# Kernel tuning notes

Hardware: AMD Instinct MI355X
Metric: run time of the kernel (lower is better)

The kernel has to match this reference:

```python
import jax, jax.numpy as jnp
import numpy as np

DIM = 1024
NUM_HEADS = 16


def setup_inputs() -> dict:
    key = jax.random.key(0)
    ks = jax.random.split(key, 7)
    B, N, C = 2, 2048, DIM
    s = 1.0 / np.sqrt(C)
    x = jax.random.normal(ks[0], (B, N, C), dtype=jnp.float32)
    Wq = jax.random.normal(ks[1], (C, C), dtype=jnp.float32) * s
    Wk = jax.random.normal(ks[2], (C, C), dtype=jnp.float32) * s
    Wv = jax.random.normal(ks[3], (C, C), dtype=jnp.float32) * s
    bq = jnp.zeros((C,), dtype=jnp.float32)
    bk = jnp.zeros((C,), dtype=jnp.float32)
    bv = jnp.zeros((C,), dtype=jnp.float32)
    return {"x": x, "Wq": Wq, "bq": bq, "Wk": Wk, "bk": bk, "Wv": Wv, "bv": bv}


def reference(x, Wq, bq, Wk, bk, Wv, bv):
    B, N, C = x.shape
    H = NUM_HEADS
    D = C // H
    # Linear projections (torch Linear: x @ W.T + b)
    q = (x @ Wq.T + bq).reshape(B, N, H, D).transpose(0, 2, 1, 3)  # [B,H,N,D]
    k = (x @ Wk.T + bk).reshape(B, N, H, D).transpose(0, 2, 1, 3)
    v = (x @ Wv.T + bv).reshape(B, N, H, D).transpose(0, 2, 1, 3)
    # NOTE: original scales by sqrt(dim)=sqrt(C), not sqrt(head_dim)
    scale = 1.0 / np.sqrt(C).astype(np.float32)
    logits = jnp.einsum('bhnd,bhmd->bhnm', q, k) * scale  # [B,H,N,N]
    attn = jax.nn.softmax(logits, axis=-1)
    out = jnp.einsum('bhnm,bhmd->bhnd', attn, v)  # [B,H,N,D]
    return out.transpose(0, 2, 1, 3).reshape(B, N, C)
```

## Files before the change

### kernel.cpp

```cpp
#include <hip/hip_runtime.h>

typedef __attribute__((ext_vector_type(8))) short bf16x8;
typedef __attribute__((ext_vector_type(4))) float f32x4;
typedef __attribute__((ext_vector_type(16))) float f32x16;
typedef __attribute__((ext_vector_type(8))) unsigned short us8;
typedef unsigned short u16;
typedef unsigned int u32;

__device__ inline u16 f2bf(float f) {
  union { float f; unsigned u; } v; v.f = f;
  unsigned r = v.u + 0x7FFFu + ((v.u >> 16) & 1u);
  return (u16)(r >> 16);
}

__device__ inline u32 cvtpk_bf16(float lo, float hi) {
  u32 r;
  asm volatile("v_cvt_pk_bf16_f32 %0, %1, %2" : "=v"(r) : "v"(lo), "v"(hi));
  return r;
}

__device__ inline void gload_lds16(const void* g, void* l) {
  __builtin_amdgcn_global_load_lds(
      (const __attribute__((address_space(1))) void*)g,
      (__attribute__((address_space(3))) void*)l, 16, 0, 0);
}

__device__ inline void p_to_pf(const f32x16& p, bf16x8& f0, bf16x8& f1) {
  union { u32 u[4]; bf16x8 v; } fr;
  u32 a = cvtpk_bf16(p[0], p[1]),   c = cvtpk_bf16(p[2], p[3]);
  u32 b = cvtpk_bf16(p[4], p[5]),   d = cvtpk_bf16(p[6], p[7]);
  asm volatile("v_permlane32_swap_b32 %0, %1" : "+v"(a), "+v"(b));
  asm volatile("v_permlane32_swap_b32 %0, %1" : "+v"(c), "+v"(d));
  fr.u[0] = a; fr.u[1] = c; fr.u[2] = b; fr.u[3] = d;  f0 = fr.v;
  u32 a2 = cvtpk_bf16(p[8], p[9]),   c2 = cvtpk_bf16(p[10], p[11]);
  u32 b2 = cvtpk_bf16(p[12], p[13]), d2 = cvtpk_bf16(p[14], p[15]);
  asm volatile("v_permlane32_swap_b32 %0, %1" : "+v"(a2), "+v"(b2));
  asm volatile("v_permlane32_swap_b32 %0, %1" : "+v"(c2), "+v"(d2));
  fr.u[0] = a2; fr.u[1] = c2; fr.u[2] = b2; fr.u[3] = d2;  f1 = fr.v;
}

__global__ void cvt_all(const float* __restrict__ x, const float* __restrict__ wq,
                        const float* __restrict__ wk, const float* __restrict__ wv,
                        u16* __restrict__ out) {
  int i = (blockIdx.x * blockDim.x + threadIdx.x) * 4;
  const float* src; int off;
  if (i < 4194304)      { src = x;  off = 0; }
  else if (i < 5242880) { src = wq; off = 4194304; }
  else if (i < 6291456) { src = wk; off = 5242880; }
  else                  { src = wv; off = 6291456; }
  float4 v = *reinterpret_cast<const float4*>(src + (i - off));
  ushort4 o;
  o.x = f2bf(v.x); o.y = f2bf(v.y); o.z = f2bf(v.z); o.w = f2bf(v.w);
  *reinterpret_cast<ushort4*>(out + i) = o;
}

__global__ __launch_bounds__(256, 3) void gemm_qkv(
    const u16* __restrict__ X,
    const u16* __restrict__ Wq, const u16* __restrict__ Wk, const u16* __restrict__ Wv,
    const float* __restrict__ bq, const float* __restrict__ bk, const float* __restrict__ bv,
    u16* __restrict__ Oq, u16* __restrict__ Ok, u16* __restrict__ Ovt)
{
  constexpr int GK = 1024;
  __shared__ __align__(16) u16 As[128 * 64];
  __shared__ __align__(16) u16 Bs[128 * 64];

  const int z = blockIdx.z;
  const u16* W = (z == 0) ? Wq : (z == 1) ? Wk : Wv;
  const float* bias = (z == 0) ? bq : (z == 1) ? bk : bv;
  const float scale = (z == 0) ? (1.4426950408889634f / 32.0f) : 1.0f;

  const int tid = threadIdx.x;
  const int lane = tid & 63, w = tid >> 6;
  const int wm = w >> 1, wn = w & 1;
  const int q = lane & 15, g = lane >> 4;
  const int bm0 = blockIdx.x * 128, bn0 = blockIdx.y * 128;

  int srow[4], sgc[4];
  #pragma unroll
  for (int i = 0; i < 4; ++i) {
    int c = i * 256 + tid;
    srow[i] = c >> 3;
    sgc[i] = (((c & 7) ^ ((c >> 3) & 7)) * 8);
  }

  f32x4 acc[4][4];
  #pragma unroll
  for (int i = 0; i < 4; ++i)
    #pragma unroll
    for (int j = 0; j < 4; ++j) acc[i][j] = (f32x4){0.f, 0.f, 0.f, 0.f};

  for (int k0 = 0; k0 < GK; k0 += 64) {
    #pragma unroll
    for (int i = 0; i < 4; ++i) {
      int c8 = (i * 256 + tid) * 8;
      gload_lds16(&X[(bm0 + srow[i]) * GK + k0 + sgc[i]], &As[c8]);
      gload_lds16(&W[(bn0 + srow[i]) * GK + k0 + sgc[i]], &Bs[c8]);
    }
    __syncthreads();

    #pragma unroll
    for (int kk = 0; kk < 2; ++kk) {
      bf16x8 af[4], bfr[4];
      #pragma unroll
      for (int mi = 0; mi < 4; ++mi) {
        int row = wm * 64 + mi * 16 + q;
        af[mi] = *reinterpret_cast<const bf16x8*>(
            &As[row * 64 + (((kk * 4 + g) ^ (row & 7)) * 8)]);
      }
      #pragma unroll
      for (int ni = 0; ni < 4; ++ni) {
        int row = wn * 64 + ni * 16 + q;
        bfr[ni] = *reinterpret_cast<const bf16x8*>(
            &Bs[row * 64 + (((kk * 4 + g) ^ (row & 7)) * 8)]);
      }
      #pragma unroll
      for (int mi = 0; mi < 4; ++mi)
        #pragma unroll
        for (int ni = 0; ni < 4; ++ni)
          acc[mi][ni] = __builtin_amdgcn_mfma_f32_16x16x32_bf16(af[mi], bfr[ni], acc[mi][ni], 0, 0, 0);
    }
    __syncthreads();
  }

  if (z == 2) {
    #pragma unroll
    for (int mi = 0; mi < 4; ++mi) {
      #pragma unroll
      for (int ni = 0; ni < 4; ++ni) {
        int col = bn0 + wn * 64 + ni * 16 + q;
        float bb = bias[col];
        int h = col >> 6, d = col & 63;
        int row0 = bm0 + wm * 64 + mi * 16 + 4 * g;
        int b = row0 >> 11, n0 = row0 & 2047;
        ushort4 o4;
        o4.x = f2bf(acc[mi][ni][0] + bb);
        o4.y = f2bf(acc[mi][ni][1] + bb);
        o4.z = f2bf(acc[mi][ni][2] + bb);
        o4.w = f2bf(acc[mi][ni][3] + bb);
        *reinterpret_cast<ushort4*>(&Ovt[(((b << 4) + h) * 64 + d) * 2048 + n0]) = o4;
      }
    }
  } else {
    u16* O = (z == 0) ? Oq : Ok;
    #pragma unroll
    for (int mi = 0; mi < 4; ++mi) {
      #pragma unroll
      for (int ni = 0; ni < 4; ++ni) {
        int col = bn0 + wn * 64 + ni * 16 + q;
        float bb = bias[col];
        int h = col >> 6, d = col & 63;
        #pragma unroll
        for (int r = 0; r < 4; ++r) {
          int row = bm0 + wm * 64 + mi * 16 + 4 * g + r;
          int b = row >> 11, n = row & 2047;
          float v = (acc[mi][ni][r] + bb) * scale;
          O[(((b << 4) + h) * 2048 + n) * 64 + d] = f2bf(v);
        }
      }
    }
  }
}

__global__ __launch_bounds__(256, 2) void attn_kernel(
    const u16* __restrict__ Q, const u16* __restrict__ K, const u16* __restrict__ Vt,
    float* __restrict__ out)
{
  __shared__ __align__(16) u16 smem[32768];

  const int tid = threadIdx.x;
  const int lane = tid & 63, w = tid >> 6;
  const int half = w >> 1, qw = w & 1;
  const int th128 = (qw << 6) + lane;
  const int ql = lane & 31, h = lane >> 5, l7 = lane & 7;

  const int lin = blockIdx.x;
  const int xcd = lin & 7, li = lin >> 3;
  const int bh = xcd * 4 + (li >> 4);
  const int b = bh >> 4, hd = bh & 15;
  const int qrow0 = (li & 15) * 128 + qw * 64;

  const u16* Qp = Q + (bh * 2048 + qrow0) * 64;
  const u16* Kp = K + (bh * 2048 + half * 1024) * 64;
  const u16* Vp = Vt + bh * 64 * 2048 + half * 1024;

  bf16x8 qf[2][4];
  #pragma unroll
  for (int qh = 0; qh < 2; ++qh)
    #pragma unroll
    for (int ks = 0; ks < 4; ++ks)
      qf[qh][ks] = *reinterpret_cast<const bf16x8*>(Qp + (qh * 32 + ql) * 64 + 16 * ks + 8 * h);

  int srow[4], scb[4];
  #pragma unroll
  for (int i = 0; i < 4; ++i) {
    int c = i * 128 + th128;
    srow[i] = c >> 3;
    scb[i] = 16 * ((c & 7) ^ ((c >> 3) & 7));
  }

  u16* Kh = smem + half * 16384;
  u16* Vh = Kh + 8192;

  f32x16 o00, o01, o10, o11;
  #pragma unroll
  for (int i = 0; i < 16; ++i) { o00[i] = 0.f; o01[i] = 0.f; o10[i] = 0.f; o11[i] = 0.f; }
  float ls0 = 0.0f, ls1 = 0.0f;

  {
    #pragma unroll
    for (int i = 0; i < 4; ++i) {
      int c8 = (i * 128 + th128) * 8;
      gload_lds16((const char*)(Kp + srow[i] * 64) + scb[i], &Kh[c8]);
      gload_lds16((const char*)(Vp + srow[i] * 2048) + scb[i], &Vh[c8]);
    }
    __syncthreads();
  }

  for (int t = 0; t < 16; ++t) {
    const int cur = t & 1, nxt = cur ^ 1;
    if (t < 15) {
      const int kbn = t * 64 + 64;
      #pragma unroll
      for (int i = 0; i < 4; ++i) {
        int c8 = (i * 128 + th128) * 8;
        gload_lds16((const char*)(Kp + (kbn + srow[i]) * 64) + scb[i], &Kh[nxt * 4096 + c8]);
        gload_lds16((const char*)(Vp + srow[i] * 2048 + kbn) + scb[i], &Vh[nxt * 4096 + c8]);
      }
    }

    f32x16 p00, p01, p10, p11;
    #pragma unroll
    for (int i = 0; i < 16; ++i) { p00[i] = 0.f; p01[i] = 0.f; p10[i] = 0.f; p11[i] = 0.f; }
    const u16* kl = Kh + cur * 4096;
    __builtin_amdgcn_s_setprio(1);
    #pragma unroll
    for (int ks = 0; ks < 4; ++ks) {
      int cb = (16 * ks + 8 * h) ^ (l7 << 3);
      bf16x8 kf0 = *reinterpret_cast<const bf16x8*>(kl + ql * 64 + cb);
      p00 = __builtin_amdgcn_mfma_f32_32x32x16_bf16(kf0, qf[0][ks], p00, 0, 0, 0);
      p01 = __builtin_amdgcn_mfma_f32_32x32x16_bf16(kf0, qf[1][ks], p01, 0, 0, 0);
      bf16x8 kf1 = *reinterpret_cast<const bf16x8*>(kl + (32 + ql) * 64 + cb);
      p10 = __builtin_amdgcn_mfma_f32_32x32x16_bf16(kf1, qf[0][ks], p10, 0, 0, 0);
      p11 = __builtin_amdgcn_mfma_f32_32x32x16_bf16(kf1, qf[1][ks], p11, 0, 0, 0);
    }
    __builtin_amdgcn_s_setprio(0);

    const u16* vl = Vh + cur * 4096;
    bf16x8 vfa[4];
    #pragma unroll
    for (int sl = 0; sl < 4; ++sl) {
      int cb = (16 * sl + 8 * h) ^ (l7 << 3);
      vfa[sl] = *reinterpret_cast<const bf16x8*>(vl + ql * 64 + cb);
    }

    #pragma unroll
    for (int i = 0; i < 16; ++i) {
      p00[i] = __builtin_amdgcn_exp2f(p00[i]);
      p01[i] = __builtin_amdgcn_exp2f(p01[i]);
      p10[i] = __builtin_amdgcn_exp2f(p10[i]);
      p11[i] = __builtin_amdgcn_exp2f(p11[i]);
    }
    {
      float s0 = 0.f, s1 = 0.f;
      #pragma unroll
      for (int i = 0; i < 16; ++i) { s0 += p00[i] + p10[i]; s1 += p01[i] + p11[i]; }
      s0 += __shfl_xor(s0, 32);
      s1 += __shfl_xor(s1, 32);
      ls0 += s0; ls1 += s1;
    }

    bf16x8 pf[4][2];
    p_to_pf(p00, pf[0][0], pf[1][0]);
    p_to_pf(p10, pf[2][0], pf[3][0]);
    p_to_pf(p01, pf[0][1], pf[1][1]);
    p_to_pf(p11, pf[2][1], pf[3][1]);

    __builtin_amdgcn_s_setprio(1);
    #pragma unroll
    for (int sl = 0; sl < 4; ++sl) {
      o00 = __builtin_amdgcn_mfma_f32_32x32x16_bf16(vfa[sl], pf[sl][0], o00, 0, 0, 0);
      o01 = __builtin_amdgcn_mfma_f32_32x32x16_bf16(vfa[sl], pf[sl][1], o01, 0, 0, 0);
      int cb = (16 * sl + 8 * h) ^ (l7 << 3);
      bf16x8 vf1 = *reinterpret_cast<const bf16x8*>(vl + (32 + ql) * 64 + cb);
      o10 = __builtin_amdgcn_mfma_f32_32x32x16_bf16(vf1, pf[sl][0], o10, 0, 0, 0);
      o11 = __builtin_amdgcn_mfma_f32_32x32x16_bf16(vf1, pf[sl][1], o11, 0, 0, 0);
    }
    __builtin_amdgcn_s_setprio(0);

    __syncthreads();
  }

  float* Of = reinterpret_cast<float*>(smem);
  float* Lf = Of + 128 * 66;
  const int obase = (qw * 64 + lane) * 66;
  if (half == 1) {
    #pragma unroll
    for (int i = 0; i < 16; ++i) {
      Of[obase + i]      = o00[i];
      Of[obase + 16 + i] = o01[i];
      Of[obase + 32 + i] = o10[i];
      Of[obase + 48 + i] = o11[i];
    }
    Lf[qw * 64 + lane] = ls0;
    Lf[128 + qw * 64 + lane] = ls1;
  }
  __syncthreads();
  if (half == 0) {
    #pragma unroll
    for (int i = 0; i < 16; ++i) {
      o00[i] += Of[obase + i];
      o01[i] += Of[obase + 16 + i];
      o10[i] += Of[obase + 32 + i];
      o11[i] += Of[obase + 48 + i];
    }
    ls0 += Lf[qw * 64 + lane];
    ls1 += Lf[128 + qw * 64 + lane];

    float r0 = 1.0f / ls0, r1 = 1.0f / ls1;
    float* op0 = out + ((size_t)(b * 2048 + qrow0 + ql) * 1024 + hd * 64);
    float* op1 = out + ((size_t)(b * 2048 + qrow0 + 32 + ql) * 1024 + hd * 64);
    #pragma unroll
    for (int g2 = 0; g2 < 4; ++g2) {
      float4 v;
      v.x = o00[4 * g2 + 0] * r0; v.y = o00[4 * g2 + 1] * r0;
      v.z = o00[4 * g2 + 2] * r0; v.w = o00[4 * g2 + 3] * r0;
      *reinterpret_cast<float4*>(op0 + 8 * g2 + 4 * h) = v;
      v.x = o10[4 * g2 + 0] * r0; v.y = o10[4 * g2 + 1] * r0;
      v.z = o10[4 * g2 + 2] * r0; v.w = o10[4 * g2 + 3] * r0;
      *reinterpret_cast<float4*>(op0 + 32 + 8 * g2 + 4 * h) = v;
      v.x = o01[4 * g2 + 0] * r1; v.y = o01[4 * g2 + 1] * r1;
      v.z = o01[4 * g2 + 2] * r1; v.w = o01[4 * g2 + 3] * r1;
      *reinterpret_cast<float4*>(op1 + 8 * g2 + 4 * h) = v;
      v.x = o11[4 * g2 + 0] * r1; v.y = o11[4 * g2 + 1] * r1;
      v.z = o11[4 * g2 + 2] * r1; v.w = o11[4 * g2 + 3] * r1;
      *reinterpret_cast<float4*>(op1 + 32 + 8 * g2 + 4 * h) = v;
    }
  }
}

extern "C" void kernel_launch(void* const* d_in, const int* in_sizes, int n_in,
                              void* d_out, int out_size, void* d_ws, size_t ws_size,
                              hipStream_t stream) {
  const float* x  = (const float*)d_in[0];
  const float* Wq = (const float*)d_in[1];
  const float* bq = (const float*)d_in[2];
  const float* Wk = (const float*)d_in[3];
  const float* bk = (const float*)d_in[4];
  const float* Wv = (const float*)d_in[5];
  const float* bv = (const float*)d_in[6];
  float* out = (float*)d_out;

  u16* ws  = (u16*)d_ws;
  u16* xb  = ws;
  u16* wqb = xb  + 4194304;
  u16* wkb = wqb + 1048576;
  u16* wvb = wkb + 1048576;
  u16* qb  = wvb + 1048576;
  u16* kb  = qb  + 4194304;
  u16* vt  = kb  + 4194304;

  cvt_all<<<7168, 256, 0, stream>>>(x, Wq, Wk, Wv, ws);

  gemm_qkv<<<dim3(32, 8, 3), 256, 0, stream>>>(xb, wqb, wkb, wvb, bq, bk, bv, qb, kb, vt);

  attn_kernel<<<512, 256, 0, stream>>>(qb, kb, vt, out);
}
```

Before: 81.68 us.

## Give each wave private double-buffered K/V tiles to drop block barriers

Previously the two waves of each half shared one 64-key K/V tile, with __syncthreads between iterations. Now each wave loads its own 32-key K/V tiles into a private LDS region, double-buffered, and waits only on its own loads via s_waitcnt vmcnt, so the loop needs no block-wide barriers. The per-iteration tile shrinks to 32 keys over 32 iterations and the V swizzle changes to a 4-way pattern. The trade-off is twice the global K/V traffic, since both query waves load the same keys, plus smaller MFMA batches per iteration and a redundant final prefetch.

```diff
diff --git a/kernel.cpp b/kernel.cpp
--- a/kernel.cpp
+++ b/kernel.cpp
@@ -170,7 +170,6 @@
   const int tid = threadIdx.x;
   const int lane = tid & 63, w = tid >> 6;
   const int half = w >> 1, qw = w & 1;
-  const int th128 = (qw << 6) + lane;
   const int ql = lane & 31, h = lane >> 5, l7 = lane & 7;
 
   const int lin = blockIdx.x;
@@ -190,106 +189,100 @@
     for (int ks = 0; ks < 4; ++ks)
       qf[qh][ks] = *reinterpret_cast<const bf16x8*>(Qp + (qh * 32 + ql) * 64 + 16 * ks + 8 * h);
 
-  int srow[4], scb[4];
+  u16* wbase = smem + w * 8192;
+  int krow_s[4], kcb_s[4], vrow_s[4], vcb_s[4];
   #pragma unroll
   for (int i = 0; i < 4; ++i) {
-    int c = i * 128 + th128;
-    srow[i] = c >> 3;
-    scb[i] = 16 * ((c & 7) ^ ((c >> 3) & 7));
-  }
-
-  u16* Kh = smem + half * 16384;
-  u16* Vh = Kh + 8192;
+    int c = i * 64 + lane;
+    krow_s[i] = c >> 3;
+    kcb_s[i] = 16 * ((c & 7) ^ ((c >> 3) & 7));
+    vrow_s[i] = c >> 2;
+    vcb_s[i] = 16 * ((c & 3) ^ ((c >> 2) & 3));
+  }
 
   f32x16 o00, o01, o10, o11;
   #pragma unroll
   for (int i = 0; i < 16; ++i) { o00[i] = 0.f; o01[i] = 0.f; o10[i] = 0.f; o11[i] = 0.f; }
   float ls0 = 0.0f, ls1 = 0.0f;
 
-  {
-    #pragma unroll
-    for (int i = 0; i < 4; ++i) {
-      int c8 = (i * 128 + th128) * 8;
-      gload_lds16((const char*)(Kp + srow[i] * 64) + scb[i], &Kh[c8]);
-      gload_lds16((const char*)(Vp + srow[i] * 2048) + scb[i], &Vh[c8]);
-    }
-    __syncthreads();
-  }
-
-  for (int t = 0; t < 16; ++t) {
+  #pragma unroll
+  for (int i = 0; i < 4; ++i)
+    gload_lds16((const char*)(Kp + krow_s[i] * 64) + kcb_s[i], &wbase[i * 512]);
+  #pragma unroll
+  for (int i = 0; i < 4; ++i)
+    gload_lds16((const char*)(Vp + vrow_s[i] * 2048) + vcb_s[i], &wbase[2048 + i * 512]);
+
+  for (int t = 0; t < 32; ++t) {
     const int cur = t & 1, nxt = cur ^ 1;
-    if (t < 15) {
-      const int kbn = t * 64 + 64;
-      #pragma unroll
-      for (int i = 0; i < 4; ++i) {
-        int c8 = (i * 128 + th128) * 8;
-        gload_lds16((const char*)(Kp + (kbn + srow[i]) * 64) + scb[i], &Kh[nxt * 4096 + c8]);
-        gload_lds16((const char*)(Vp + srow[i] * 2048 + kbn) + scb[i], &Vh[nxt * 4096 + c8]);
-      }
-    }
-
-    f32x16 p00, p01, p10, p11;
-    #pragma unroll
-    for (int i = 0; i < 16; ++i) { p00[i] = 0.f; p01[i] = 0.f; p10[i] = 0.f; p11[i] = 0.f; }
-    const u16* kl = Kh + cur * 4096;
+    const int kb = t * 32;
+    const int kbn = (t < 31) ? (kb + 32) : kb;
+    u16* nb = wbase + nxt * 4096;
+    #pragma unroll
+    for (int i = 0; i < 4; ++i)
+      gload_lds16((const char*)(Kp + (kbn + krow_s[i]) * 64) + kcb_s[i], &nb[i * 512]);
+    #pragma unroll
+    for (int i = 0; i < 4; ++i)
+      gload_lds16((const char*)(Vp + vrow_s[i] * 2048 + kbn) + vcb_s[i], &nb[2048 + i * 512]);
+
+    asm volatile("s_waitcnt vmcnt(8)" ::: "memory");
+    __builtin_amdgcn_sched_barrier(0);
+
+    const u16* kl = wbase + cur * 4096;
+    const u16* vl = kl + 2048;
+
+    f32x16 p0, p1;
+    #pragma unroll
+    for (int i = 0; i < 16; ++i) { p0[i] = 0.f; p1[i] = 0.f; }
     __builtin_amdgcn_s_setprio(1);
     #pragma unroll
     for (int ks = 0; ks < 4; ++ks) {
-      int cb = (16 * ks + 8 * h) ^ (l7 << 3);
-      bf16x8 kf0 = *reinterpret_cast<const bf16x8*>(kl + ql * 64 + cb);
-      p00 = __builtin_amdgcn_mfma_f32_32x32x16_bf16(kf0, qf[0][ks], p00, 0, 0, 0);
-      p01 = __builtin_amdgcn_mfma_f32_32x32x16_bf16(kf0, qf[1][ks], p01, 0, 0, 0);
-      bf16x8 kf1 = *reinterpret_cast<const bf16x8*>(kl + (32 + ql) * 64 + cb);
-      p10 = __builtin_amdgcn_mfma_f32_32x32x16_bf16(kf1, qf[0][ks], p10, 0, 0, 0);
-      p11 = __builtin_amdgcn_mfma_f32_32x32x16_bf16(kf1, qf[1][ks], p11, 0, 0, 0);
+      bf16x8 kf = *reinterpret_cast<const bf16x8*>(
+          kl + ql * 64 + (((2 * ks + h) ^ (ql & 7)) * 8));
+      p0 = __builtin_amdgcn_mfma_f32_32x32x16_bf16(kf, qf[0][ks], p0, 0, 0, 0);
+      p1 = __builtin_amdgcn_mfma_f32_32x32x16_bf16(kf, qf[1][ks], p1, 0, 0, 0);
     }
     __builtin_amdgcn_s_setprio(0);
 
-    const u16* vl = Vh + cur * 4096;
-    bf16x8 vfa[4];
-    #pragma unroll
-    for (int sl = 0; sl < 4; ++sl) {
-      int cb = (16 * sl + 8 * h) ^ (l7 << 3);
-      vfa[sl] = *reinterpret_cast<const bf16x8*>(vl + ql * 64 + cb);
-    }
+    bf16x8 vf[2][2];
+    #pragma unroll
+    for (int dt = 0; dt < 2; ++dt)
+      #pragma unroll
+      for (int kss = 0; kss < 2; ++kss) {
+        int r = dt * 32 + ql;
+        vf[dt][kss] = *reinterpret_cast<const bf16x8*>(
+            vl + r * 32 + (((2 * kss + h) ^ (r & 3)) * 8));
+      }
 
     #pragma unroll
     for (int i = 0; i < 16; ++i) {
-      p00[i] = __builtin_amdgcn_exp2f(p00[i]);
-      p01[i] = __builtin_amdgcn_exp2f(p01[i]);
-      p10[i] = __builtin_amdgcn_exp2f(p10[i]);
-      p11[i] = __builtin_amdgcn_exp2f(p11[i]);
+      p0[i] = __builtin_amdgcn_exp2f(p0[i]);
+      p1[i] = __builtin_amdgcn_exp2f(p1[i]);
     }
     {
       float s0 = 0.f, s1 = 0.f;
       #pragma unroll
-      for (int i = 0; i < 16; ++i) { s0 += p00[i] + p10[i]; s1 += p01[i] + p11[i]; }
+      for (int i = 0; i < 16; ++i) { s0 += p0[i]; s1 += p1[i]; }
       s0 += __shfl_xor(s0, 32);
       s1 += __shfl_xor(s1, 32);
       ls0 += s0; ls1 += s1;
     }
 
-    bf16x8 pf[4][2];
-    p_to_pf(p00, pf[0][0], pf[1][0]);
-    p_to_pf(p10, pf[2][0], pf[3][0]);
-    p_to_pf(p01, pf[0][1], pf[1][1]);
-    p_to_pf(p11, pf[2][1], pf[3][1]);
+    bf16x8 pf0[2], pf1[2];
+    p_to_pf(p0, pf0[0], pf0[1]);
+    p_to_pf(p1, pf1[0], pf1[1]);
 
     __builtin_amdgcn_s_setprio(1);
     #pragma unroll
-    for (int sl = 0; sl < 4; ++sl) {
-      o00 = __builtin_amdgcn_mfma_f32_32x32x16_bf16(vfa[sl], pf[sl][0], o00, 0, 0, 0);
-      o01 = __builtin_amdgcn_mfma_f32_32x32x16_bf16(vfa[sl], pf[sl][1], o01, 0, 0, 0);
-      int cb = (16 * sl + 8 * h) ^ (l7 << 3);
-      bf16x8 vf1 = *reinterpret_cast<const bf16x8*>(vl + (32 + ql) * 64 + cb);
-      o10 = __builtin_amdgcn_mfma_f32_32x32x16_bf16(vf1, pf[sl][0], o10, 0, 0, 0);
-      o11 = __builtin_amdgcn_mfma_f32_32x32x16_bf16(vf1, pf[sl][1], o11, 0, 0, 0);
+    for (int kss = 0; kss < 2; ++kss) {
+      o00 = __builtin_amdgcn_mfma_f32_32x32x16_bf16(vf[0][kss], pf0[kss], o00, 0, 0, 0);
+      o01 = __builtin_amdgcn_mfma_f32_32x32x16_bf16(vf[0][kss], pf1[kss], o01, 0, 0, 0);
+      o10 = __builtin_amdgcn_mfma_f32_32x32x16_bf16(vf[1][kss], pf0[kss], o10, 0, 0, 0);
+      o11 = __builtin_amdgcn_mfma_f32_32x32x16_bf16(vf[1][kss], pf1[kss], o11, 0, 0, 0);
     }
     __builtin_amdgcn_s_setprio(0);
-
-    __syncthreads();
-  }
-
+  }
+
+  __syncthreads();
   float* Of = reinterpret_cast<float*>(smem);
   float* Lf = Of + 128 * 66;
   const int obase = (qw * 64 + lane) * 66;
```

After: 87.80 us. 7.5% more time.
